# Optimization experiments

Measured on AMD Instinct MI355X. Metric: run time of the kernel, lower is better.

## Reference

```python
import jax, jax.numpy as jnp
import numpy as np

D = 1024          # model_dim
BD = D // 2       # bottleneck_dim
K = 64            # num_splats
B, S = 8, 2048


def setup_inputs() -> dict:
    key = jax.random.key(0)
    ks = jax.random.split(key, 12)
    sc = 0.02
    return {
        "token_embeddings": jax.random.normal(ks[0], (B, S, D), jnp.float32),
        "splat_influences": jax.random.uniform(ks[1], (B, S, K), jnp.float32),
        # encoder: Linear(D -> BD), stored [in, out]
        "enc_W": jax.random.normal(ks[2], (D, BD), jnp.float32) * sc,
        "enc_b": jnp.zeros((BD,), jnp.float32),
        # per-splat transforms: K x Linear(BD -> BD)
        "trans_W": jax.random.normal(ks[3], (K, BD, BD), jnp.float32) * sc,
        "trans_b": jnp.zeros((K, BD), jnp.float32),
        # decoder: Linear(BD -> D)
        "dec_W": jax.random.normal(ks[4], (BD, D), jnp.float32) * sc,
        "dec_b": jnp.zeros((D,), jnp.float32),
        # flow gate: Linear(D -> D) + sigmoid
        "gate_W": jax.random.normal(ks[5], (D, D), jnp.float32) * sc,
        "gate_b": jnp.zeros((D,), jnp.float32),
    }


def reference(token_embeddings, splat_influences, enc_W, enc_b,
              trans_W, trans_b, dec_W, dec_b, gate_W, gate_b):
    # gather: [B,K,S] @ [B,S,D] -> [B,K,D]
    influences_t = jnp.swapaxes(splat_influences, 1, 2)          # [B,K,S]
    gathered = jnp.einsum('bks,bsd->bkd', influences_t, token_embeddings)
    total = jnp.clip(influences_t.sum(axis=2, keepdims=True), 1e-8, None)  # [B,K,1]
    gathered = gathered / total
    # encoder (dropout inactive at eval)
    encoded = jax.nn.relu(gathered @ enc_W + enc_b)              # [B,K,BD]
    # per-splat transform as grouped matmul
    transformed = jnp.einsum('bkd,kde->bke', encoded, trans_W) + trans_b  # [B,K,BD]
    decoded = transformed @ dec_W + dec_b                        # [B,K,D]
    # scatter back to tokens: [B,S,K] @ [B,K,D]
    flow = jnp.einsum('bsk,bkd->bsd', splat_influences, decoded)
    gate = jax.nn.sigmoid(token_embeddings @ gate_W + gate_b)    # [B,S,D]
    return flow * gate
```

## Files before the change

kernel.cpp:

```cpp
#include <hip/hip_runtime.h>

#define BB 8
#define SS 2048
#define DD 1024
#define BDD 512
#define NSP 64

typedef __attribute__((ext_vector_type(8))) short bf16x8;
typedef __attribute__((ext_vector_type(4))) float f32x4;
typedef unsigned short u16;
typedef unsigned int u32;

__device__ __forceinline__ u16 f2bf(float f) {
  u32 u = __builtin_bit_cast(u32, f);
  u = u + 0x7fffu + ((u >> 16) & 1u);
  return (u16)(u >> 16);
}

__device__ __forceinline__ void gl_lds16(const void* g, void* l) {
  __builtin_amdgcn_global_load_lds((const __attribute__((address_space(1))) void*)g,
                                   (__attribute__((address_space(3))) void*)l,
                                   16, 0, 0);
}

__global__ void k_prep(const float* __restrict__ tok, const float* __restrict__ infl,
                       const float* __restrict__ gw, u16* __restrict__ tokbf,
                       u16* __restrict__ tokT, u16* __restrict__ inflbf,
                       u16* __restrict__ inflT, float* __restrict__ rsum,
                       u16* __restrict__ gwt) {
  __shared__ __align__(16) char smraw[64 * 80 * 2 + 32 * 64 * 4];
  u16(*tile)[80] = (u16(*)[80])smraw;
  float(*ps)[64] = (float(*)[64])(smraw + 64 * 80 * 2);
  float(*gt)[33] = (float(*)[33])smraw;
  int bid = blockIdx.x;
  int t = threadIdx.x;

  if (bid < 4096) {
    int C0 = (bid & 15) * 64;
    int R0 = (bid >> 4) * 64;
    int b = R0 >> 11, s0 = R0 & 2047;
    int lr = t >> 3, lc = (t & 7) * 8;
#pragma unroll
    for (int i = 0; i < 2; ++i) {
      int r = lr + i * 32;
      const float* src = tok + (size_t)(R0 + r) * DD + C0 + lc;
      float4 a = *(const float4*)src;
      float4 bq = *(const float4*)(src + 4);
      uint4 v;
      v.x = f2bf(a.x) | ((u32)f2bf(a.y) << 16);
      v.y = f2bf(a.z) | ((u32)f2bf(a.w) << 16);
      v.z = f2bf(bq.x) | ((u32)f2bf(bq.y) << 16);
      v.w = f2bf(bq.z) | ((u32)f2bf(bq.w) << 16);
      *(uint4*)(tokbf + (size_t)(R0 + r) * DD + C0 + lc) = v;
      *(uint4*)&tile[r][lc] = v;
    }
    __syncthreads();
    int sseg = (t & 7) * 8;
#pragma unroll
    for (int i = 0; i < 2; ++i) {
      int dcol = (t >> 3) + i * 32;
      u16 a0 = tile[sseg + 0][dcol], a1 = tile[sseg + 1][dcol];
      u16 a2 = tile[sseg + 2][dcol], a3 = tile[sseg + 3][dcol];
      u16 a4 = tile[sseg + 4][dcol], a5 = tile[sseg + 5][dcol];
      u16 a6 = tile[sseg + 6][dcol], a7 = tile[sseg + 7][dcol];
      uint4 v;
      v.x = a0 | ((u32)a1 << 16);
      v.y = a2 | ((u32)a3 << 16);
      v.z = a4 | ((u32)a5 << 16);
      v.w = a6 | ((u32)a7 << 16);
      *(uint4*)(tokT + (size_t)b * DD * SS + (size_t)(C0 + dcol) * SS + s0 + sseg) = v;
    }
  } else if (bid < 4352) {
    int R0 = (bid - 4096) * 64;
    int b = R0 >> 11, s0 = R0 & 2047;
    int st = s0 >> 6;
    int lr = t >> 3, lc = (t & 7) * 8;
    float col[8];
#pragma unroll
    for (int j = 0; j < 8; ++j) col[j] = 0.f;
#pragma unroll
    for (int i = 0; i < 2; ++i) {
      int r = lr + i * 32;
      const float* src = infl + (size_t)(R0 + r) * NSP + lc;
      float4 a = *(const float4*)src;
      float4 bq = *(const float4*)(src + 4);
      col[0] += a.x; col[1] += a.y; col[2] += a.z; col[3] += a.w;
      col[4] += bq.x; col[5] += bq.y; col[6] += bq.z; col[7] += bq.w;
      uint4 v;
      v.x = f2bf(a.x) | ((u32)f2bf(a.y) << 16);
      v.y = f2bf(a.z) | ((u32)f2bf(a.w) << 16);
      v.z = f2bf(bq.x) | ((u32)f2bf(bq.y) << 16);
      v.w = f2bf(bq.z) | ((u32)f2bf(bq.w) << 16);
      *(uint4*)(inflbf + (size_t)(R0 + r) * NSP + lc) = v;
      *(uint4*)&tile[r][lc] = v;
    }
#pragma unroll
    for (int j = 0; j < 8; ++j) ps[lr][lc + j] = col[j];
    __syncthreads();
    if (t < 64) {
      float s = 0.f;
#pragma unroll
      for (int rr = 0; rr < 32; ++rr) s += ps[rr][t];
      rsum[((size_t)b * 32 + st) * 64 + t] = s;
    }
    int sseg = (t & 7) * 8;
#pragma unroll
    for (int i = 0; i < 2; ++i) {
      int dcol = (t >> 3) + i * 32;
      u16 a0 = tile[sseg + 0][dcol], a1 = tile[sseg + 1][dcol];
      u16 a2 = tile[sseg + 2][dcol], a3 = tile[sseg + 3][dcol];
      u16 a4 = tile[sseg + 4][dcol], a5 = tile[sseg + 5][dcol];
      u16 a6 = tile[sseg + 6][dcol], a7 = tile[sseg + 7][dcol];
      uint4 v;
      v.x = a0 | ((u32)a1 << 16);
      v.y = a2 | ((u32)a3 << 16);
      v.z = a4 | ((u32)a5 << 16);
      v.w = a6 | ((u32)a7 << 16);
      *(uint4*)(inflT + ((size_t)b * NSP + dcol) * SS + s0 + sseg) = v;
    }
  } else {
    int g = bid - 4352;
    int n0 = (g & 31) * 32, k0 = (g >> 5) * 32;
    int tx = t & 31, ty = t >> 5;
#pragma unroll
    for (int r = 0; r < 4; ++r) {
      int kr = ty + r * 8;
      gt[kr][tx] = gw[(k0 + kr) * DD + n0 + tx];
    }
    __syncthreads();
#pragma unroll
    for (int r = 0; r < 4; ++r) {
      int nc = ty + r * 8;
      gwt[(n0 + nc) * DD + k0 + tx] = f2bf(gt[tx][nc]);
    }
  }
}

__global__ __launch_bounds__(256) void k_gather_mfma(const u16* __restrict__ inflT,
                                                     const u16* __restrict__ tokT,
                                                     float* __restrict__ pg) {
  __shared__ u16 As[64 * 64];
  __shared__ u16 Bs[64 * 64];
  int t = threadIdx.x;
  int l = t & 63, w = t >> 6;
  int wr = w >> 1, wc = w & 1;
  int n0 = blockIdx.x * 64;
  int b = blockIdx.y;
  int sq = blockIdx.z;
  int l15 = l & 15, lh = l >> 4;
  int srow = t >> 3, scol = (t & 7) * 8;

  const u16* ap = inflT + (size_t)b * NSP * SS;
  const u16* bp = tokT + (size_t)b * DD * SS;

  f32x4 acc[2][2];
#pragma unroll
  for (int i = 0; i < 2; ++i)
#pragma unroll
    for (int j = 0; j < 2; ++j) acc[i][j] = (f32x4){0.f, 0.f, 0.f, 0.f};

  for (int kt = 0; kt < 8; ++kt) {
    int k0 = sq * 512 + kt * 64;
#pragma unroll
    for (int i = 0; i < 2; ++i) {
      int row = srow + i * 32;
      gl_lds16(ap + row * SS + k0 + scol, &As[row * 64 + scol]);
      gl_lds16(bp + (n0 + row) * SS + k0 + scol, &Bs[row * 64 + scol]);
    }
    __syncthreads();
#pragma unroll
    for (int ks = 0; ks < 2; ++ks) {
      bf16x8 af[2], bfv[2];
#pragma unroll
      for (int mi = 0; mi < 2; ++mi)
        af[mi] = *(const bf16x8*)&As[(wr * 32 + mi * 16 + l15) * 64 + ks * 32 + lh * 8];
#pragma unroll
      for (int ni = 0; ni < 2; ++ni)
        bfv[ni] = *(const bf16x8*)&Bs[(wc * 32 + ni * 16 + l15) * 64 + ks * 32 + lh * 8];
#pragma unroll
      for (int mi = 0; mi < 2; ++mi)
#pragma unroll
        for (int ni = 0; ni < 2; ++ni)
          acc[mi][ni] = __builtin_amdgcn_mfma_f32_16x16x32_bf16(af[mi], bfv[ni], acc[mi][ni], 0, 0, 0);
    }
    __syncthreads();
  }

#pragma unroll
  for (int mi = 0; mi < 2; ++mi)
#pragma unroll
    for (int ni = 0; ni < 2; ++ni)
#pragma unroll
      for (int r = 0; r < 4; ++r) {
        int krow = wr * 32 + mi * 16 + lh * 4 + r;
        int dcol = n0 + wc * 32 + ni * 16 + l15;
        pg[((size_t)sq * 512 + b * NSP + krow) * DD + dcol] = acc[mi][ni][r];
      }
}

__global__ void k_enc_part(const float* __restrict__ pg, const float* __restrict__ rsum,
                           const float* __restrict__ encW, float* __restrict__ pe) {
  __shared__ float gl[8][64];
  int dq = blockIdx.x, mt = blockIdx.y;
  int m0 = mt * 8, d0 = dq * 64;
  int t = threadIdx.x;
  {
    int r = t >> 5, c = t & 31;
    float s1 = 0.f, s2 = 0.f;
#pragma unroll
    for (int q = 0; q < 4; ++q) {
      const float* qp = pg + ((size_t)q * 512 + m0 + r) * DD + d0;
      s1 += qp[c]; s2 += qp[c + 32];
    }
    int mrow = m0 + r;
    int bq = mrow >> 6, kq = mrow & 63;
    float tt = 0.f;
#pragma unroll
    for (int st = 0; st < 32; ++st) tt += rsum[((size_t)bq * 32 + st) * 64 + kq];
    float rt = 1.f / fmaxf(tt, 1e-8f);
    gl[r][c] = s1 * rt;
    gl[r][c + 32] = s2 * rt;
  }
  __syncthreads();
  int n4 = (t & 127) * 4, mh = (t >> 7) * 4;
  float4 acc[4];
#pragma unroll
  for (int m = 0; m < 4; ++m) acc[m] = (float4){0.f, 0.f, 0.f, 0.f};
  for (int i = 0; i < 64; ++i) {
    float4 wv = *(const float4*)(encW + (d0 + i) * BDD + n4);
#pragma unroll
    for (int m = 0; m < 4; ++m) {
      float g = gl[mh + m][i];
      acc[m].x += g * wv.x; acc[m].y += g * wv.y;
      acc[m].z += g * wv.z; acc[m].w += g * wv.w;
    }
  }
#pragma unroll
  for (int m = 0; m < 4; ++m)
    *(float4*)(pe + ((size_t)dq * 512 + m0 + mh + m) * BDD + n4) = acc[m];
}

__global__ void k_trans_part(const float* __restrict__ pe, const float* __restrict__ encB,
                             const float* __restrict__ trW, float* __restrict__ pt) {
  __shared__ float el[8][32];
  int dq = blockIdx.x, ks = blockIdx.y;
  int d0 = dq * 32;
  int t = threadIdx.x;
  {
    int r = t >> 5, c = t & 31;
    int m = r * NSP + ks;
    float s = 0.f;
#pragma unroll
    for (int p = 0; p < 16; ++p)
      s += pe[((size_t)p * 512 + m) * BDD + d0 + c];
    el[r][c] = fmaxf(s + encB[d0 + c], 0.f);
  }
  __syncthreads();
  int n4 = (t & 127) * 4, mh = (t >> 7) * 4;
  float4 acc[4];
#pragma unroll
  for (int m = 0; m < 4; ++m) acc[m] = (float4){0.f, 0.f, 0.f, 0.f};
  for (int i = 0; i < 32; ++i) {
    float4 wv = *(const float4*)(trW + ((size_t)ks * BDD + d0 + i) * BDD + n4);
#pragma unroll
    for (int m = 0; m < 4; ++m) {
      float g = el[mh + m][i];
      acc[m].x += g * wv.x; acc[m].y += g * wv.y;
      acc[m].z += g * wv.z; acc[m].w += g * wv.w;
    }
  }
#pragma unroll
  for (int m = 0; m < 4; ++m)
    *(float4*)(pt + ((size_t)dq * 512 + (mh + m) * NSP + ks) * BDD + n4) = acc[m];
}

__global__ void k_dec_part(const float* __restrict__ pt, const float* __restrict__ trB,
                           const float* __restrict__ decW, float* __restrict__ pd) {
  __shared__ float tl[8][64];
  int dq = blockIdx.x, mt = blockIdx.y;
  int m0 = mt * 8, d0 = dq * 64;
  int t = threadIdx.x;
  {
    int r = t >> 5, c = t & 31;
    int m = m0 + r;
    float s1 = 0.f, s2 = 0.f;
#pragma unroll
    for (int p = 0; p < 16; ++p) {
      const float* qp = pt + ((size_t)p * 512 + m) * BDD + d0;
      s1 += qp[c]; s2 += qp[c + 32];
    }
    tl[r][c] = s1 + trB[(m & 63) * BDD + d0 + c];
    tl[r][c + 32] = s2 + trB[(m & 63) * BDD + d0 + c + 32];
  }
  __syncthreads();
  int n4 = t * 4;
  float4 acc[8];
#pragma unroll
  for (int m = 0; m < 8; ++m) acc[m] = (float4){0.f, 0.f, 0.f, 0.f};
  for (int i = 0; i < 64; ++i) {
    float4 wv = *(const float4*)(decW + (d0 + i) * DD + n4);
#pragma unroll
    for (int m = 0; m < 8; ++m) {
      float g = tl[m][i];
      acc[m].x += g * wv.x; acc[m].y += g * wv.y;
      acc[m].z += g * wv.z; acc[m].w += g * wv.w;
    }
  }
#pragma unroll
  for (int m = 0; m < 8; ++m)
    *(float4*)(pd + ((size_t)dq * 512 + m0 + m) * DD + n4) = acc[m];
}

__global__ void red_dec(const float* __restrict__ pd, const float* __restrict__ decB,
                        u16* __restrict__ decT) {
  __shared__ u16 st[64][34];
  int nt = blockIdx.x, b = blockIdx.y;
  int n0 = nt * 32;
  int t = threadIdx.x;
  int nn = t & 31, kg = t >> 5;
  float db = decB[n0 + nn];
#pragma unroll
  for (int ki = 0; ki < 8; ++ki) {
    int ks = kg * 8 + ki;
    float s = db;
#pragma unroll
    for (int p = 0; p < 8; ++p)
      s += pd[((size_t)p * 512 + b * NSP + ks) * DD + n0 + nn];
    st[ks][nn] = f2bf(s);
  }
  __syncthreads();
  int nr = t >> 3, kseg = (t & 7) * 8;
  uint4 v;
  v.x = st[kseg + 0][nr] | ((u32)st[kseg + 1][nr] << 16);
  v.y = st[kseg + 2][nr] | ((u32)st[kseg + 3][nr] << 16);
  v.z = st[kseg + 4][nr] | ((u32)st[kseg + 5][nr] << 16);
  v.w = st[kseg + 6][nr] | ((u32)st[kseg + 7][nr] << 16);
  *(uint4*)(decT + ((size_t)b * DD + n0 + nr) * NSP + kseg) = v;
}


#define GVM(n) asm volatile("s_waitcnt vmcnt(" #n ")" ::: "memory");

#define GSTA(sl, k0, p)                                                        \
  { int e = (p)*512 + t; int row = e >> 3; int cs = ((e & 7) ^ (row & 7)) * 8; \
    gl_lds16(tokbf + (size_t)(m0 + row) * DD + (k0) + cs, &As[sl][e * 8]); }
#define GSTB(sl, k0, p)                                                        \
  { int e = (p)*512 + t; int row = e >> 3; int cs = ((e & 7) ^ (row & 7)) * 8; \
    gl_lds16(gwt + (size_t)(n0 + row) * DD + (k0) + cs, &Bs[sl][e * 8]); }

#define GLOADB(sl)                                                             \
  _Pragma("unroll")                                                            \
  for (int nf = 0; nf < 2; ++nf) {                                             \
    int br = wc * 32 + nf * 16 + l15;                                          \
    bfv[nf][0] = *(const bf16x8*)&Bs[sl][br * 64 + c0];                        \
    bfv[nf][1] = *(const bf16x8*)&Bs[sl][br * 64 + c1];                        \
  }

#define GPH(sl, mq, VMW, STG, LDB)                                             \
  {                                                                            \
    VMW                                                                        \
    __builtin_amdgcn_s_barrier();                                              \
    LDB                                                                        \
    bf16x8 af[4][2];                                                           \
    _Pragma("unroll")                                                          \
    for (int mf = 0; mf < 4; ++mf) {                                           \
      int ar = (mq)*64 + mf * 16 + l15;                                        \
      af[mf][0] = *(const bf16x8*)&As[sl][ar * 64 + c0];                       \
      af[mf][1] = *(const bf16x8*)&As[sl][ar * 64 + c1];                       \
    }                                                                          \
    STG                                                                        \
    __builtin_amdgcn_s_setprio(1);                                             \
    _Pragma("unroll")                                                          \
    for (int mf = 0; mf < 4; ++mf)                                             \
      _Pragma("unroll")                                                        \
      for (int nf = 0; nf < 2; ++nf) {                                         \
        acc[(mq)*4 + mf][nf] = __builtin_amdgcn_mfma_f32_16x16x32_bf16(af[mf][0], bfv[nf][0], acc[(mq)*4 + mf][nf], 0, 0, 0); \
        acc[(mq)*4 + mf][nf] = __builtin_amdgcn_mfma_f32_16x16x32_bf16(af[mf][1], bfv[nf][1], acc[(mq)*4 + mf][nf], 0, 0, 0); \
      }                                                                        \
    __builtin_amdgcn_s_setprio(0);                                             \
    __builtin_amdgcn_s_barrier();                                              \
  }

#define GT_FULL(sl, osl, k1)                                                   \
  {                                                                            \
    bf16x8 bfv[2][2];                                                          \
    GPH(sl, 0, GVM(3), GSTB(osl, k1, 0) GSTB(osl, k1, 1), GLOADB(sl))          \
    GPH(sl, 1, GVM(4), GSTB(osl, k1, 2) GSTB(osl, k1, 3), )                    \
    GPH(sl, 2, GVM(5), GSTA(osl, k1, 0) GSTA(osl, k1, 1), )                    \
    GPH(sl, 3, GVM(6), GSTA(osl, k1, 2) GSTA(osl, k1, 3), )                    \
  }
#define GT_LAST(sl)                                                            \
  {                                                                            \
    bf16x8 bfv[2][2];                                                          \
    GPH(sl, 0, GVM(3), , GLOADB(sl))                                           \
    GPH(sl, 1, GVM(2), , )                                                     \
    GPH(sl, 2, GVM(1), , )                                                     \
    GPH(sl, 3, GVM(0), , )                                                     \
  }

__global__ __launch_bounds__(512, 2) void k_gate(const u16* __restrict__ tokbf,
                                                 const u16* __restrict__ gwt,
                                                 u16* __restrict__ zbf) {
  __shared__ u16 As[2][256 * 64];
  __shared__ u16 Bs[2][256 * 64];
  int t = threadIdx.x;
  int l = t & 63, wc = t >> 6;
  int bid = blockIdx.x;
  int wg = (bid & 7) * 32 + (bid >> 3);
  int mt = wg & 63, nt = wg >> 6;
  int m0 = mt * 256, n0 = nt * 256;
  int l15 = l & 15, lh = l >> 4;
  int x7 = l15 & 7;
  int c0 = (lh ^ x7) * 8;
  int c1 = ((4 + lh) ^ x7) * 8;

  f32x4 acc[16][2];
#pragma unroll
  for (int i = 0; i < 16; ++i)
#pragma unroll
    for (int j = 0; j < 2; ++j) acc[i][j] = (f32x4){0.f, 0.f, 0.f, 0.f};

  GSTB(0, 0, 0) GSTB(0, 0, 1) GSTB(0, 0, 2) GSTB(0, 0, 3)
  GSTA(0, 0, 0) GSTA(0, 0, 1) GSTA(0, 0, 2) GSTA(0, 0, 3)

#pragma unroll 1
  for (int i = 0; i < 7; ++i) {
    GT_FULL(0, 1, (2 * i + 1) * 64)
    GT_FULL(1, 0, (2 * i + 2) * 64)
  }
  GT_FULL(0, 1, 960)
  GT_LAST(1)

#pragma unroll
  for (int a = 0; a < 16; ++a)
#pragma unroll
    for (int nf = 0; nf < 2; ++nf)
#pragma unroll
      for (int r = 0; r < 4; ++r) {
        int mr = m0 + a * 16 + lh * 4 + r;
        int nc = n0 + wc * 32 + nf * 16 + l15;
        zbf[(size_t)mr * DD + nc] = f2bf(acc[a][nf][r]);
      }
}

__global__ __launch_bounds__(256) void k_scat(const u16* __restrict__ inflbf,
                                              const u16* __restrict__ decT,
                                              const u16* __restrict__ zbf,
                                              const float* __restrict__ gateB,
                                              float* __restrict__ outp) {
  __shared__ u16 As[128 * 64];
  __shared__ u16 Bs[128 * 64];
  int t = threadIdx.x;
  int l = t & 63, w = t >> 6;
  int wr = w >> 1, wc = w & 1;
  int m0 = blockIdx.x * 128, n0 = blockIdx.y * 128;
  int l15 = l & 15, lh = l >> 4;
  int b = m0 >> 11, s0m = m0 & 2047;

#pragma unroll
  for (int i = 0; i < 4; ++i) {
    int row = i * 32 + (t >> 3);
    int cs = ((t & 7) ^ (row & 7)) * 8;
    gl_lds16(inflbf + ((size_t)b * SS + s0m + row) * NSP + cs, &As[i * 2048 + t * 8]);
  }
#pragma unroll
  for (int i = 0; i < 4; ++i) {
    int row = i * 32 + (t >> 3);
    int cs = ((t & 7) ^ (row & 7)) * 8;
    gl_lds16(decT + ((size_t)b * DD + n0 + row) * NSP + cs, &Bs[i * 2048 + t * 8]);
  }
  asm volatile("s_waitcnt vmcnt(0)" ::: "memory");
  __builtin_amdgcn_s_barrier();

  f32x4 accf[4][4];
#pragma unroll
  for (int i = 0; i < 4; ++i)
#pragma unroll
    for (int j = 0; j < 4; ++j) accf[i][j] = (f32x4){0.f, 0.f, 0.f, 0.f};
#pragma unroll
  for (int ks = 0; ks < 2; ++ks) {
    bf16x8 af[4], bfv[4];
    int g = ks * 4 + lh;
#pragma unroll
    for (int mi = 0; mi < 4; ++mi) {
      int r = wr * 64 + mi * 16 + l15;
      af[mi] = *(const bf16x8*)&As[r * 64 + (g ^ (r & 7)) * 8];
    }
#pragma unroll
    for (int ni = 0; ni < 4; ++ni) {
      int r = wc * 64 + ni * 16 + l15;
      bfv[ni] = *(const bf16x8*)&Bs[r * 64 + (g ^ (r & 7)) * 8];
    }
#pragma unroll
    for (int mi = 0; mi < 4; ++mi)
#pragma unroll
      for (int ni = 0; ni < 4; ++ni)
        accf[mi][ni] = __builtin_amdgcn_mfma_f32_16x16x32_bf16(af[mi], bfv[ni], accf[mi][ni], 0, 0, 0);
  }

  float gb[4];
#pragma unroll
  for (int ni = 0; ni < 4; ++ni) gb[ni] = gateB[n0 + wc * 64 + ni * 16 + l15];
#pragma unroll
  for (int mi = 0; mi < 4; ++mi)
#pragma unroll
    for (int ni = 0; ni < 4; ++ni)
#pragma unroll
      for (int r = 0; r < 4; ++r) {
        int mr = m0 + wr * 64 + mi * 16 + lh * 4 + r;
        int nc = n0 + wc * 64 + ni * 16 + l15;
        u16 zr = zbf[(size_t)mr * DD + nc];
        float z = __builtin_bit_cast(float, (u32)zr << 16) + gb[ni];
        float gate = 1.f / (1.f + __expf(-z));
        outp[(size_t)mr * DD + nc] = accf[mi][ni][r] * gate;
      }
}

extern "C" void kernel_launch(void* const* d_in, const int* in_sizes, int n_in,
                              void* d_out, int out_size, void* d_ws, size_t ws_size,
                              hipStream_t stream) {
  const float* tok = (const float*)d_in[0];
  const float* infl = (const float*)d_in[1];
  const float* encW = (const float*)d_in[2];
  const float* encB = (const float*)d_in[3];
  const float* trW = (const float*)d_in[4];
  const float* trB = (const float*)d_in[5];
  const float* decW = (const float*)d_in[6];
  const float* decB = (const float*)d_in[7];
  const float* gw = (const float*)d_in[8];
  const float* gateB = (const float*)d_in[9];
  float* outp = (float*)d_out;

  char* wsp = (char*)d_ws;
  u16* tokbf = (u16*)(wsp);
  u16* gwt = (u16*)(wsp + 33554432);
  u16* inflbf = (u16*)(wsp + 35651584);
  u16* decT = (u16*)(wsp + 41945088);
  u16* tokT = (u16*)(wsp + 42993664);
  float* pe = (float*)(wsp + 42993664);
  float* pt = (float*)(wsp + 42993664 + 16777216);
  u16* zbf = (u16*)(wsp + 42993664);
  u16* inflT = (u16*)(wsp + 76548096);
  float* rsum = (float*)(wsp + 78645248);
  float* scratch = (float*)(wsp + 78710784);

  k_prep<<<dim3(5376), dim3(256), 0, stream>>>(tok, infl, gw, tokbf, tokT, inflbf,
                                               inflT, rsum, gwt);
  k_gather_mfma<<<dim3(16, 8, 4), dim3(256), 0, stream>>>(inflT, tokT, scratch);
  k_enc_part<<<dim3(16, 64), dim3(256), 0, stream>>>(scratch, rsum, encW, pe);
  k_trans_part<<<dim3(16, 64), dim3(256), 0, stream>>>(pe, encB, trW, pt);
  k_dec_part<<<dim3(8, 64), dim3(256), 0, stream>>>(pt, trB, decW, scratch);
  red_dec<<<dim3(32, 8), dim3(256), 0, stream>>>(scratch, decB, decT);
  k_gate<<<dim3(256), dim3(512), 0, stream>>>(tokbf, gwt, zbf);
  k_scat<<<dim3(128, 8), dim3(256), 0, stream>>>(inflbf, decT, zbf, gateB, outp);
}
```

Measured before the change: 172.2 us.

## Shrink gate GEMM tiles to 128x256xK32 and pad prep transpose LDS

```diff
diff --git a/kernel.cpp b/kernel.cpp
--- a/kernel.cpp
+++ b/kernel.cpp
@@ -36,6 +36,7 @@
   int t = threadIdx.x;
 
   if (bid < 4096) {
+    u32* t32 = (u32*)smraw;
     int C0 = (bid & 15) * 64;
     int R0 = (bid >> 4) * 64;
     int b = R0 >> 11, s0 = R0 & 2047;
@@ -52,24 +53,30 @@
       v.z = f2bf(bq.x) | ((u32)f2bf(bq.y) << 16);
       v.w = f2bf(bq.z) | ((u32)f2bf(bq.w) << 16);
       *(uint4*)(tokbf + (size_t)(R0 + r) * DD + C0 + lc) = v;
-      *(uint4*)&tile[r][lc] = v;
+      int cbase = r * 41 + (t & 7) * 4;
+      t32[cbase + 0] = v.x;
+      t32[cbase + 1] = v.y;
+      t32[cbase + 2] = v.z;
+      t32[cbase + 3] = v.w;
     }
     __syncthreads();
+    int dp = t >> 3;
     int sseg = (t & 7) * 8;
-#pragma unroll
-    for (int i = 0; i < 2; ++i) {
-      int dcol = (t >> 3) + i * 32;
-      u16 a0 = tile[sseg + 0][dcol], a1 = tile[sseg + 1][dcol];
-      u16 a2 = tile[sseg + 2][dcol], a3 = tile[sseg + 3][dcol];
-      u16 a4 = tile[sseg + 4][dcol], a5 = tile[sseg + 5][dcol];
-      u16 a6 = tile[sseg + 6][dcol], a7 = tile[sseg + 7][dcol];
-      uint4 v;
-      v.x = a0 | ((u32)a1 << 16);
-      v.y = a2 | ((u32)a3 << 16);
-      v.z = a4 | ((u32)a5 << 16);
-      v.w = a6 | ((u32)a7 << 16);
-      *(uint4*)(tokT + (size_t)b * DD * SS + (size_t)(C0 + dcol) * SS + s0 + sseg) = v;
-    }
+    u32 w[8];
+#pragma unroll
+    for (int j = 0; j < 8; ++j) w[j] = t32[(sseg + j) * 41 + dp];
+    uint4 vlo, vhi;
+    vlo.x = (w[0] & 0xffffu) | (w[1] << 16);
+    vlo.y = (w[2] & 0xffffu) | (w[3] << 16);
+    vlo.z = (w[4] & 0xffffu) | (w[5] << 16);
+    vlo.w = (w[6] & 0xffffu) | (w[7] << 16);
+    vhi.x = (w[0] >> 16) | (w[1] & 0xffff0000u);
+    vhi.y = (w[2] >> 16) | (w[3] & 0xffff0000u);
+    vhi.z = (w[4] >> 16) | (w[5] & 0xffff0000u);
+    vhi.w = (w[6] >> 16) | (w[7] & 0xffff0000u);
+    size_t tb = (size_t)b * DD * SS;
+    *(uint4*)(tokT + tb + (size_t)(C0 + 2 * dp) * SS + s0 + sseg) = vlo;
+    *(uint4*)(tokT + tb + (size_t)(C0 + 2 * dp + 1) * SS + s0 + sseg) = vhi;
   } else if (bid < 4352) {
     int R0 = (bid - 4096) * 64;
     int b = R0 >> 11, s0 = R0 & 2047;
@@ -339,100 +346,98 @@
 }
 
 
-#define GVM(n) asm volatile("s_waitcnt vmcnt(" #n ")" ::: "memory");
-
-#define GSTA(sl, k0, p)                                                        \
-  { int e = (p)*512 + t; int row = e >> 3; int cs = ((e & 7) ^ (row & 7)) * 8; \
-    gl_lds16(tokbf + (size_t)(m0 + row) * DD + (k0) + cs, &As[sl][e * 8]); }
-#define GSTB(sl, k0, p)                                                        \
-  { int e = (p)*512 + t; int row = e >> 3; int cs = ((e & 7) ^ (row & 7)) * 8; \
+#define GVM1 asm volatile("s_waitcnt vmcnt(1)" ::: "memory");
+#define GVM0 asm volatile("s_waitcnt vmcnt(0)" ::: "memory");
+
+#define STA32(sl, k0)                                                         \
+  { int row = t >> 2; int cs = (((t & 3) ^ (row & 3)) << 3);                  \
+    gl_lds16(tokbf + (size_t)(m0 + row) * DD + (k0) + cs, &As[sl][t * 8]); }
+#define STB32(sl, k0, p)                                                      \
+  { int e = (p)*512 + t; int row = e >> 2; int cs = (((e & 3) ^ (row & 3)) << 3); \
     gl_lds16(gwt + (size_t)(n0 + row) * DD + (k0) + cs, &Bs[sl][e * 8]); }
 
-#define GLOADB(sl)                                                             \
-  _Pragma("unroll")                                                            \
-  for (int nf = 0; nf < 2; ++nf) {                                             \
-    int br = wc * 32 + nf * 16 + l15;                                          \
-    bfv[nf][0] = *(const bf16x8*)&Bs[sl][br * 64 + c0];                        \
-    bfv[nf][1] = *(const bf16x8*)&Bs[sl][br * 64 + c1];                        \
-  }
-
-#define GPH(sl, mq, VMW, STG, LDB)                                             \
-  {                                                                            \
-    VMW                                                                        \
-    __builtin_amdgcn_s_barrier();                                              \
-    LDB                                                                        \
-    bf16x8 af[4][2];                                                           \
-    _Pragma("unroll")                                                          \
-    for (int mf = 0; mf < 4; ++mf) {                                           \
-      int ar = (mq)*64 + mf * 16 + l15;                                        \
-      af[mf][0] = *(const bf16x8*)&As[sl][ar * 64 + c0];                       \
-      af[mf][1] = *(const bf16x8*)&As[sl][ar * 64 + c1];                       \
-    }                                                                          \
-    STG                                                                        \
-    __builtin_amdgcn_s_setprio(1);                                             \
-    _Pragma("unroll")                                                          \
-    for (int mf = 0; mf < 4; ++mf)                                             \
-      _Pragma("unroll")                                                        \
-      for (int nf = 0; nf < 2; ++nf) {                                         \
-        acc[(mq)*4 + mf][nf] = __builtin_amdgcn_mfma_f32_16x16x32_bf16(af[mf][0], bfv[nf][0], acc[(mq)*4 + mf][nf], 0, 0, 0); \
-        acc[(mq)*4 + mf][nf] = __builtin_amdgcn_mfma_f32_16x16x32_bf16(af[mf][1], bfv[nf][1], acc[(mq)*4 + mf][nf], 0, 0, 0); \
-      }                                                                        \
-    __builtin_amdgcn_s_setprio(0);                                             \
-    __builtin_amdgcn_s_barrier();                                              \
-  }
-
-#define GT_FULL(sl, osl, k1)                                                   \
-  {                                                                            \
-    bf16x8 bfv[2][2];                                                          \
-    GPH(sl, 0, GVM(3), GSTB(osl, k1, 0) GSTB(osl, k1, 1), GLOADB(sl))          \
-    GPH(sl, 1, GVM(4), GSTB(osl, k1, 2) GSTB(osl, k1, 3), )                    \
-    GPH(sl, 2, GVM(5), GSTA(osl, k1, 0) GSTA(osl, k1, 1), )                    \
-    GPH(sl, 3, GVM(6), GSTA(osl, k1, 2) GSTA(osl, k1, 3), )                    \
-  }
-#define GT_LAST(sl)                                                            \
-  {                                                                            \
-    bf16x8 bfv[2][2];                                                          \
-    GPH(sl, 0, GVM(3), , GLOADB(sl))                                           \
-    GPH(sl, 1, GVM(2), , )                                                     \
-    GPH(sl, 2, GVM(1), , )                                                     \
-    GPH(sl, 3, GVM(0), , )                                                     \
-  }
-
-__global__ __launch_bounds__(512, 2) void k_gate(const u16* __restrict__ tokbf,
+#define GLOADB32(sl)                                                          \
+  _Pragma("unroll")                                                           \
+  for (int nf = 0; nf < 2; ++nf) {                                            \
+    int br = wc * 32 + nf * 16 + l15;                                         \
+    bfv[nf] = *(const bf16x8*)&Bs[sl][br * 32 + ((lh ^ (br & 3)) << 3)];      \
+  }
+#define GFRAGA(sl, mq)                                                        \
+  _Pragma("unroll")                                                           \
+  for (int mf = 0; mf < 4; ++mf) {                                            \
+    int ar = (mq)*64 + mf * 16 + l15;                                         \
+    af[mf] = *(const bf16x8*)&As[sl][ar * 32 + ((lh ^ (ar & 3)) << 3)];       \
+  }
+#define GMFMA(mq)                                                             \
+  __builtin_amdgcn_s_setprio(1);                                              \
+  _Pragma("unroll")                                                           \
+  for (int mf = 0; mf < 4; ++mf)                                              \
+    _Pragma("unroll")                                                         \
+    for (int nf = 0; nf < 2; ++nf)                                            \
+      acc[(mq)*4 + mf][nf] = __builtin_amdgcn_mfma_f32_16x16x32_bf16(af[mf], bfv[nf], acc[(mq)*4 + mf][nf], 0, 0, 0); \
+  __builtin_amdgcn_s_setprio(0);
+
+#define GT32(sl, osl, k1)                                                     \
+  { bf16x8 bfv[2], af[4];                                                     \
+    STB32(osl, k1, 0)                                                         \
+    GVM1                                                                      \
+    __builtin_amdgcn_s_barrier();                                             \
+    GLOADB32(sl)                                                              \
+    GFRAGA(sl, 0)                                                             \
+    GMFMA(0)                                                                  \
+    __builtin_amdgcn_s_barrier();                                             \
+    STB32(osl, k1, 1)                                                         \
+    STA32(osl, k1)                                                            \
+    GFRAGA(sl, 1)                                                             \
+    GMFMA(1)                                                                  \
+    __builtin_amdgcn_s_barrier(); }
+
+#define GT32L(sl)                                                             \
+  { bf16x8 bfv[2], af[4];                                                     \
+    GVM0                                                                      \
+    __builtin_amdgcn_s_barrier();                                             \
+    GLOADB32(sl)                                                              \
+    GFRAGA(sl, 0)                                                             \
+    GMFMA(0)                                                                  \
+    __builtin_amdgcn_s_barrier();                                             \
+    GFRAGA(sl, 1)                                                             \
+    GMFMA(1)                                                                  \
+    __builtin_amdgcn_s_barrier(); }
+
+__global__ __launch_bounds__(512, 4) void k_gate(const u16* __restrict__ tokbf,
                                                  const u16* __restrict__ gwt,
                                                  u16* __restrict__ zbf) {
-  __shared__ u16 As[2][256 * 64];
-  __shared__ u16 Bs[2][256 * 64];
+  __shared__ u16 As[2][128 * 32];
+  __shared__ u16 Bs[2][256 * 32];
   int t = threadIdx.x;
   int l = t & 63, wc = t >> 6;
   int bid = blockIdx.x;
-  int wg = (bid & 7) * 32 + (bid >> 3);
-  int mt = wg & 63, nt = wg >> 6;
-  int m0 = mt * 256, n0 = nt * 256;
+  int idx = bid >> 3;
+  int mt = (bid & 7) * 16 + (idx & 15);
+  int nt = idx >> 4;
+  int m0 = mt * 128, n0 = nt * 256;
   int l15 = l & 15, lh = l >> 4;
-  int x7 = l15 & 7;
-  int c0 = (lh ^ x7) * 8;
-  int c1 = ((4 + lh) ^ x7) * 8;
-
-  f32x4 acc[16][2];
-#pragma unroll
-  for (int i = 0; i < 16; ++i)
+
+  f32x4 acc[8][2];
+#pragma unroll
+  for (int i = 0; i < 8; ++i)
 #pragma unroll
     for (int j = 0; j < 2; ++j) acc[i][j] = (f32x4){0.f, 0.f, 0.f, 0.f};
 
-  GSTB(0, 0, 0) GSTB(0, 0, 1) GSTB(0, 0, 2) GSTB(0, 0, 3)
-  GSTA(0, 0, 0) GSTA(0, 0, 1) GSTA(0, 0, 2) GSTA(0, 0, 3)
+  STB32(0, 0, 0)
+  STB32(0, 0, 1)
+  STA32(0, 0)
 
 #pragma unroll 1
-  for (int i = 0; i < 7; ++i) {
-    GT_FULL(0, 1, (2 * i + 1) * 64)
-    GT_FULL(1, 0, (2 * i + 2) * 64)
-  }
-  GT_FULL(0, 1, 960)
-  GT_LAST(1)
-
-#pragma unroll
-  for (int a = 0; a < 16; ++a)
+  for (int i = 0; i < 15; ++i) {
+    GT32(0, 1, (2 * i + 1) * 32)
+    GT32(1, 0, (2 * i + 2) * 32)
+  }
+  GT32(0, 1, 992)
+  GT32L(1)
+
+#pragma unroll
+  for (int a = 0; a < 8; ++a)
 #pragma unroll
     for (int nf = 0; nf < 2; ++nf)
 #pragma unroll
@@ -551,6 +556,6 @@
   k_trans_part<<<dim3(16, 64), dim3(256), 0, stream>>>(pe, encB, trW, pt);
   k_dec_part<<<dim3(8, 64), dim3(256), 0, stream>>>(pt, trB, decW, scratch);
   red_dec<<<dim3(32, 8), dim3(256), 0, stream>>>(scratch, decB, decT);
-  k_gate<<<dim3(256), dim3(512), 0, stream>>>(tokbf, gwt, zbf);
+  k_gate<<<dim3(512), dim3(512), 0, stream>>>(tokbf, gwt, zbf);
   k_scat<<<dim3(128, 8), dim3(256), 0, stream>>>(inflbf, decT, zbf, gateB, outp);
 }
```

Result: slower. 176.8 us (+2.7%).
